# Kernel optimization log

Measured on AMD Instinct MI355X. Metric: run time of the kernel, lower is better.

Reference implementation:

```python
import jax, jax.numpy as jnp
import numpy as np

ALPHA = 0.2  # leaky relu slope
NEG_INF = -9e15  # matches torch constant -9000000000000000.0


def setup_inputs() -> dict:
    key = jax.random.key(0)
    k1, k2, k3, k4, k5 = jax.random.split(key, 5)
    B, S, FIN, FOUT, H = 1, 4096, 128, 64, 8
    input_seq = jax.random.normal(k1, (B, S, FIN), dtype=jnp.float32)
    adj = jax.random.randint(k2, (B, S, S), 0, 2, dtype=jnp.int32)
    W = jax.random.normal(k3, (H, FIN, FOUT), dtype=jnp.float32) * 0.1
    a_1 = jax.random.normal(k4, (H, FOUT, 1), dtype=jnp.float32) * 0.1
    a_2 = jax.random.normal(k5, (H, FOUT, 1), dtype=jnp.float32) * 0.1
    return {"input_seq": input_seq, "adj": adj, "W": W, "a_1": a_1, "a_2": a_2}


def reference(input_seq, adj, W, a_1, a_2):
    B, S, _ = input_seq.shape
    H, _, FOUT = W.shape
    # h: [B, H, S, FOUT]
    h = jnp.einsum('bni,hio->bhno', input_seq, W)
    f1 = jnp.einsum('bhno,hoz->bhnz', h, a_1)[..., 0]  # [B,H,S]
    f2 = jnp.einsum('bhno,hoz->bhnz', h, a_2)[..., 0]  # [B,H,S]
    # e[b,h,i,j] = f1[i] + f2[j]
    e = jax.nn.leaky_relu(f1[:, :, :, None] + f2[:, :, None, :], ALPHA)
    mask = adj[:, None, :, :] > 0  # [B,1,S,S] broadcast over heads
    e = jnp.where(mask, e, NEG_INF)
    # NOTE: original softmax is over dim=2 (source-node axis), not -1
    attention = jax.nn.softmax(e, axis=2)
    # dropout is inference-mode no-op
    node_out = jnp.einsum('bhij,bhjo->bhio', attention, h)  # [B,H,S,FOUT]
    node_out = jnp.transpose(node_out, (0, 2, 1, 3)).reshape(B, S, H * FOUT)
    node_out = jax.nn.elu(node_out)
    return jnp.squeeze(node_out)
```

## Files before the change

kernel.cpp:

```cpp
#include <hip/hip_runtime.h>

#define S 4096
#define FIN 128
#define FOUT 64
#define H 8
#define ALPHA 0.2f

typedef __attribute__((ext_vector_type(2)))  _Float16 f16x2;
typedef __attribute__((ext_vector_type(8)))  _Float16 f16x8;
typedef __attribute__((ext_vector_type(16))) float    f32x16;

__device__ __forceinline__ unsigned short f2h(float x) {
    return __builtin_bit_cast(unsigned short, (_Float16)x);
}

__global__ __launch_bounds__(256) void k_proj(const float* __restrict__ X,
                                              const float* __restrict__ W,
                                              const float* __restrict__ a1,
                                              const float* __restrict__ a2,
                                              unsigned short* __restrict__ hT,
                                              float2* __restrict__ E1h,
                                              float2* __restrict__ E2p) {
    __shared__ float xs[64][36];
    __shared__ float Ws[32][68];
    const int h  = blockIdx.y;
    const int j0 = blockIdx.x * 64;
    const int t  = threadIdx.x;
    const int fg = t & 15, rg = t >> 4;
    const int jr = t >> 2, q = t & 3;
    const int kw = t >> 3, cw = t & 7;
    float acc[4][4] = {};
#pragma unroll
    for (int k0 = 0; k0 < FIN; k0 += 32) {
        *(float4*)&xs[jr][q * 8]      = *(const float4*)&X[(j0 + jr) * FIN + k0 + q * 8];
        *(float4*)&xs[jr][q * 8 + 4]  = *(const float4*)&X[(j0 + jr) * FIN + k0 + q * 8 + 4];
        *(float4*)&Ws[kw][cw * 8]     = *(const float4*)&W[(h * FIN + k0 + kw) * FOUT + cw * 8];
        *(float4*)&Ws[kw][cw * 8 + 4] = *(const float4*)&W[(h * FIN + k0 + kw) * FOUT + cw * 8 + 4];
        __syncthreads();
#pragma unroll
        for (int kc = 0; kc < 8; ++kc) {
            float4 xr[4], wr[4];
#pragma unroll
            for (int r = 0; r < 4; ++r) xr[r] = *(const float4*)&xs[4 * rg + r][kc * 4];
#pragma unroll
            for (int kk = 0; kk < 4; ++kk) wr[kk] = *(const float4*)&Ws[kc * 4 + kk][fg * 4];
#pragma unroll
            for (int r = 0; r < 4; ++r) {
                const float* xp = (const float*)&xr[r];
#pragma unroll
                for (int kk = 0; kk < 4; ++kk) {
                    const float xv = xp[kk];
                    acc[r][0] += xv * wr[kk].x;
                    acc[r][1] += xv * wr[kk].y;
                    acc[r][2] += xv * wr[kk].z;
                    acc[r][3] += xv * wr[kk].w;
                }
            }
        }
        __syncthreads();
    }
    const float4 a1v = *(const float4*)&a1[h * FOUT + fg * 4];
    const float4 a2v = *(const float4*)&a2[h * FOUT + fg * 4];
#pragma unroll
    for (int r = 0; r < 4; ++r) {
        float p1 = acc[r][0] * a1v.x + acc[r][1] * a1v.y + acc[r][2] * a1v.z + acc[r][3] * a1v.w;
        float p2 = acc[r][0] * a2v.x + acc[r][1] * a2v.y + acc[r][2] * a2v.z + acc[r][3] * a2v.w;
#pragma unroll
        for (int off = 1; off < 16; off <<= 1) {
            p1 += __shfl_xor(p1, off, 64);
            p2 += __shfl_xor(p2, off, 64);
        }
        if (fg == 0) {
            const int row = j0 + 4 * rg + r;
            E1h[(size_t)row * H + h] = make_float2(__expf(p1), __expf(ALPHA * p1));
            E2p[h * S + row]         = make_float2(__expf(p2), __expf(ALPHA * p2));
        }
    }
#pragma unroll
    for (int c = 0; c < 4; ++c) {
        ushort4 pk;
        pk.x = f2h(acc[0][c]);
        pk.y = f2h(acc[1][c]);
        pk.z = f2h(acc[2][c]);
        pk.w = f2h(acc[3][c]);
        *(ushort4*)&hT[(h * FOUT + fg * 4 + c) * S + j0 + 4 * rg] = pk;
    }
}

__global__ __launch_bounds__(256) void k_colsum(const int* __restrict__ adj,
                                                const float2* __restrict__ E1h,
                                                const float2* __restrict__ E2p,
                                                float* __restrict__ Dcol,
                                                unsigned int* __restrict__ bm) {
    __shared__ float red[4][H][64];
    const int j0    = blockIdx.x * 64;
    const int ibase = blockIdx.y * 256;
    const int t  = threadIdx.x;
    const int jl = t & 63;
    const int wv = __builtin_amdgcn_readfirstlane(t >> 6);
    float2 e2v[H];
    float Dl[H];
#pragma unroll
    for (int hh = 0; hh < H; ++hh) { e2v[hh] = E2p[hh * S + j0 + jl]; Dl[hh] = 0.f; }
    const int rowbase = ibase + wv * 64;
    for (int s = 0; s < 64; ++s) {
        const int row = rowbase + s;
        const float2* __restrict__ e1r = E1h + (size_t)row * H;
        const int av = adj[(size_t)row * S + j0 + jl];
        const unsigned long long blt = __ballot(av != 0);
        if (jl == 0)
            *(uint2*)&bm[row * (S / 32) + (j0 >> 5)] =
                make_uint2((unsigned int)blt, (unsigned int)(blt >> 32));
        const float bf = av != 0 ? 1.f : 0.f;
#pragma unroll
        for (int hh = 0; hh < H; ++hh) {
            const float2 e1 = e1r[hh];
            Dl[hh] = fmaf(bf, fmaxf(e1.x * e2v[hh].x, e1.y * e2v[hh].y), Dl[hh]);
        }
    }
#pragma unroll
    for (int hh = 0; hh < H; ++hh) red[wv][hh][jl] = Dl[hh];
    __syncthreads();
    if (wv == 0) {
#pragma unroll
        for (int hh = 0; hh < H; ++hh) {
            const float sum = red[0][hh][jl] + red[1][hh][jl] +
                              red[2][hh][jl] + red[3][hh][jl];
            atomicAdd(&Dcol[hh * S + j0 + jl], sum);
        }
    }
}

__global__ __launch_bounds__(256) void k_finish(const float* __restrict__ Dcol,
                                                const float2* __restrict__ E2p,
                                                uint2* __restrict__ wE2h) {
    const int idx = blockIdx.x * 256 + threadIdx.x;
    const int hh = idx >> 11, p = idx & 2047;
    const int j = 2 * p;
    const float2 a  = E2p[hh * S + j];
    const float2 b  = E2p[hh * S + j + 1];
    const float  wa = 1.0f / Dcol[hh * S + j];
    const float  wb = 1.0f / Dcol[hh * S + j + 1];
    f16x2 qx, qy;
    qx[0] = (_Float16)(a.x * wa); qx[1] = (_Float16)(b.x * wb);
    qy[0] = (_Float16)(a.y * wa); qy[1] = (_Float16)(b.y * wb);
    wE2h[idx] = make_uint2(__builtin_bit_cast(unsigned int, qx),
                           __builtin_bit_cast(unsigned int, qy));
}

__global__ __launch_bounds__(512, 4) void k_attn(const unsigned int* __restrict__ bm,
                                                 const float2* __restrict__ E1h,
                                                 const uint2* __restrict__ wE2h,
                                                 const unsigned short* __restrict__ hT,
                                                 float* __restrict__ out) {
    __shared__ __align__(16) char smem[65536];
    const int h  = blockIdx.y;
    const int i0 = blockIdx.x * 64;
    const int t  = threadIdx.x;
    const int lane = t & 63, wv = t >> 6;
    const int q = wv >> 1, mw = wv & 1;
    const int am = lane & 31, kh = lane >> 5;
    const int i  = i0 + mw * 32 + am;
    const int tq = t & 127;
    const int sf = tq >> 1;
    const int sc = (tq & 1) * 4;
    unsigned short* B0 = (unsigned short*)(smem + q * 16384);
    unsigned short* B1 = B0 + 4096;
    const int jbase = q * 1024;

    const float2 e1 = E1h[(size_t)i * H + h];
    f16x2 ea2, eb2;
    ea2[0] = ea2[1] = (_Float16)e1.x;
    eb2[0] = eb2[1] = (_Float16)e1.y;

    f32x16 acc0 = {0,0,0,0,0,0,0,0,0,0,0,0,0,0,0,0};
    f32x16 acc1 = {0,0,0,0,0,0,0,0,0,0,0,0,0,0,0,0};

    const unsigned short* hrow  = hT + ((h * FOUT + sf) * S) + jbase + sc * 8;
    const unsigned int*   bmrow = bm + (size_t)i * (S / 32) + (jbase >> 5);
    const uint2*          e2b   = wE2h + h * (S / 2) + (jbase >> 1) + kh * 4;

    {
        const uint4* sp = (const uint4*)hrow;
        const uint4 v0 = sp[0], v1 = sp[1], v2 = sp[2], v3 = sp[3];
        *(uint4*)(B0 + sf * 64 + (((sc + 0) ^ (sf & 7)) * 8)) = v0;
        *(uint4*)(B0 + sf * 64 + (((sc + 1) ^ (sf & 7)) * 8)) = v1;
        *(uint4*)(B0 + sf * 64 + (((sc + 2) ^ (sf & 7)) * 8)) = v2;
        *(uint4*)(B0 + sf * 64 + (((sc + 3) ^ (sf & 7)) * 8)) = v3;
    }
    uint2 mrn = *(const uint2*)bmrow;
    __syncthreads();

    for (int jt = 0; jt < 16; ++jt) {
        unsigned short* Bc = (jt & 1) ? B1 : B0;
        unsigned short* Bn = (jt & 1) ? B0 : B1;
        const uint2 mr = mrn;
        if (jt < 15) {
            const uint4* sp = (const uint4*)(hrow + (jt + 1) * 64);
            const uint4 v0 = sp[0], v1 = sp[1], v2 = sp[2], v3 = sp[3];
            *(uint4*)(Bn + sf * 64 + (((sc + 0) ^ (sf & 7)) * 8)) = v0;
            *(uint4*)(Bn + sf * 64 + (((sc + 1) ^ (sf & 7)) * 8)) = v1;
            *(uint4*)(Bn + sf * 64 + (((sc + 2) ^ (sf & 7)) * 8)) = v2;
            *(uint4*)(Bn + sf * 64 + (((sc + 3) ^ (sf & 7)) * 8)) = v3;
            mrn = *(const uint2*)(bmrow + (jt + 1) * 2);
        }
        const unsigned int sh = kh * 8;
        unsigned int bys[4];
        bys[0] = (mr.x >> sh) & 0xffu;
        bys[1] = (mr.x >> (sh + 16)) & 0xffu;
        bys[2] = (mr.y >> sh) & 0xffu;
        bys[3] = (mr.y >> (sh + 16)) & 0xffu;
#pragma unroll
        for (int s = 0; s < 4; ++s) {
            const uint4 eA = *(const uint4*)(e2b + jt * 32 + s * 8);
            const uint4 eB = *(const uint4*)(e2b + jt * 32 + s * 8 + 2);
            const unsigned int by = bys[s];
            uint4 aw;
#define GAT_PAIR(pp, qxu, qyu, dst)                                               \
            {                                                                     \
                const f16x2 pa = ea2 * __builtin_bit_cast(f16x2, qxu);            \
                const f16x2 pb = eb2 * __builtin_bit_cast(f16x2, qyu);            \
                const unsigned int pm = __builtin_bit_cast(unsigned int,          \
                    __builtin_elementwise_max(pa, pb));                           \
                const unsigned int t2 = (by >> (2 * pp)) & 3u;                    \
                const unsigned int msk = ((0u - (t2 & 1u)) & 0xFFFFu) |           \
                                         ((0u - (t2 >> 1)) << 16);                \
                dst = pm & msk;                                                   \
            }
            GAT_PAIR(0, eA.x, eA.y, aw.x)
            GAT_PAIR(1, eA.z, eA.w, aw.y)
            GAT_PAIR(2, eB.x, eB.y, aw.z)
            GAT_PAIR(3, eB.z, eB.w, aw.w)
#undef GAT_PAIR
            const int chunk = s * 2 + kh;
            const f16x8 a  = __builtin_bit_cast(f16x8, aw);
            const f16x8 b0 = *(const f16x8*)(Bc + am * 64 + ((chunk ^ (am & 7)) * 8));
            const f16x8 b1 = *(const f16x8*)(Bc + (am + 32) * 64 + ((chunk ^ (am & 7)) * 8));
            acc0 = __builtin_amdgcn_mfma_f32_32x32x16_f16(a, b0, acc0, 0, 0, 0);
            acc1 = __builtin_amdgcn_mfma_f32_32x32x16_f16(a, b1, acc1, 0, 0, 0);
        }
        __syncthreads();
    }

    float* r1 = (float*)smem;
    float* r3 = (float*)(smem + 18432);
    const int ro = (mw * 64 + lane) * 36;
    if (q == 1) {
#pragma unroll
        for (int r = 0; r < 16; ++r) { r1[ro + r] = acc0[r]; r1[ro + 16 + r] = acc1[r]; }
    }
    if (q == 3) {
#pragma unroll
        for (int r = 0; r < 16; ++r) { r3[ro + r] = acc0[r]; r3[ro + 16 + r] = acc1[r]; }
    }
    __syncthreads();
    if (q == 0) {
#pragma unroll
        for (int r = 0; r < 16; ++r) { acc0[r] += r1[ro + r]; acc1[r] += r1[ro + 16 + r]; }
    }
    if (q == 2) {
#pragma unroll
        for (int r = 0; r < 16; ++r) { acc0[r] += r3[ro + r]; acc1[r] += r3[ro + 16 + r]; }
    }
    __syncthreads();
    if (q == 2) {
#pragma unroll
        for (int r = 0; r < 16; ++r) { r1[ro + r] = acc0[r]; r1[ro + 16 + r] = acc1[r]; }
    }
    __syncthreads();
    if (q == 0) {
#pragma unroll
        for (int r = 0; r < 16; ++r) { acc0[r] += r1[ro + r]; acc1[r] += r1[ro + 16 + r]; }
#pragma unroll
        for (int r = 0; r < 16; ++r) {
            const int il  = (r & 3) + 8 * (r >> 2) + 4 * kh;
            const int row = i0 + mw * 32 + il;
            const float x0 = acc0[r], x1 = acc1[r];
            out[row * (H * FOUT) + h * FOUT + am]      = x0 > 0.f ? x0 : __expf(x0) - 1.f;
            out[row * (H * FOUT) + h * FOUT + 32 + am] = x1 > 0.f ? x1 : __expf(x1) - 1.f;
        }
    }
}

extern "C" void kernel_launch(void* const* d_in, const int* in_sizes, int n_in,
                              void* d_out, int out_size, void* d_ws, size_t ws_size,
                              hipStream_t stream) {
    const float* X   = (const float*)d_in[0];
    const int*   adj = (const int*)d_in[1];
    const float* W   = (const float*)d_in[2];
    const float* a1  = (const float*)d_in[3];
    const float* a2  = (const float*)d_in[4];
    float* out = (float*)d_out;

    char* ws = (char*)d_ws;
    unsigned short* hT   = (unsigned short*)ws;
    float2*         E1h  = (float2*)(ws + 4194304);
    float2*         E2p  = (float2*)(ws + 4456448);
    float*          Dcol = (float*)(ws + 4718592);
    uint2*          wE2h = (uint2*)(ws + 4849664);
    unsigned int*   bm   = (unsigned int*)(ws + 4980736);

    (void)hipMemsetAsync(Dcol, 0, H * S * sizeof(float), stream);
    k_proj  <<<dim3(S / 64, H),       256, 0, stream>>>(X, W, a1, a2, hT, E1h, E2p);
    k_colsum<<<dim3(S / 64, S / 256), 256, 0, stream>>>(adj, E1h, E2p, Dcol, bm);
    k_finish<<<dim3(H * S / 512),     256, 0, stream>>>(Dcol, E2p, wE2h);
    k_attn  <<<dim3(S / 64, H),       512, 0, stream>>>(bm, E1h, wE2h, hT, out);
}
```

Baseline: 211.5 us.

## Fuse normalization into attention kernel, drop atomics, load B operands directly

Removes the memset and the k_finish kernel. k_colsum now writes per-block partial column sums instead of atomics, and k_attn reduces those 16 partials per column into shared memory at its start. The adjacency bitmask is stored transposed so each lane's mask loads coalesce across rows. The hT tile is no longer staged through double-buffered LDS with barriers; MFMA B operands are read straight from global memory with a padded row stride. This saves launches, atomics and per-tile syncs, but every attention block now redoes the normalization reduction and relies on the cache to serve the uncoalesced B-operand loads.

```diff
diff --git a/kernel.cpp b/kernel.cpp
--- a/kernel.cpp
+++ b/kernel.cpp
@@ -1,6 +1,7 @@
 #include <hip/hip_runtime.h>
 
 #define S 4096
+#define PS 4128
 #define FIN 128
 #define FOUT 64
 #define H 8
@@ -83,15 +84,15 @@
         pk.y = f2h(acc[1][c]);
         pk.z = f2h(acc[2][c]);
         pk.w = f2h(acc[3][c]);
-        *(ushort4*)&hT[(h * FOUT + fg * 4 + c) * S + j0 + 4 * rg] = pk;
+        *(ushort4*)&hT[(size_t)(h * FOUT + fg * 4 + c) * PS + j0 + 4 * rg] = pk;
     }
 }
 
 __global__ __launch_bounds__(256) void k_colsum(const int* __restrict__ adj,
                                                 const float2* __restrict__ E1h,
                                                 const float2* __restrict__ E2p,
-                                                float* __restrict__ Dcol,
-                                                unsigned int* __restrict__ bm) {
+                                                float* __restrict__ Dpart,
+                                                unsigned int* __restrict__ bmT) {
     __shared__ float red[4][H][64];
     const int j0    = blockIdx.x * 64;
     const int ibase = blockIdx.y * 256;
@@ -108,9 +109,10 @@
         const float2* __restrict__ e1r = E1h + (size_t)row * H;
         const int av = adj[(size_t)row * S + j0 + jl];
         const unsigned long long blt = __ballot(av != 0);
-        if (jl == 0)
-            *(uint2*)&bm[row * (S / 32) + (j0 >> 5)] =
-                make_uint2((unsigned int)blt, (unsigned int)(blt >> 32));
+        if (jl == 0) {
+            bmT[(j0 >> 5) * S + row]       = (unsigned int)blt;
+            bmT[((j0 >> 5) + 1) * S + row] = (unsigned int)(blt >> 32);
+        }
         const float bf = av != 0 ? 1.f : 0.f;
 #pragma unroll
         for (int hh = 0; hh < H; ++hh) {
@@ -126,46 +128,47 @@
         for (int hh = 0; hh < H; ++hh) {
             const float sum = red[0][hh][jl] + red[1][hh][jl] +
                               red[2][hh][jl] + red[3][hh][jl];
-            atomicAdd(&Dcol[hh * S + j0 + jl], sum);
-        }
-    }
-}
-
-__global__ __launch_bounds__(256) void k_finish(const float* __restrict__ Dcol,
-                                                const float2* __restrict__ E2p,
-                                                uint2* __restrict__ wE2h) {
-    const int idx = blockIdx.x * 256 + threadIdx.x;
-    const int hh = idx >> 11, p = idx & 2047;
-    const int j = 2 * p;
-    const float2 a  = E2p[hh * S + j];
-    const float2 b  = E2p[hh * S + j + 1];
-    const float  wa = 1.0f / Dcol[hh * S + j];
-    const float  wb = 1.0f / Dcol[hh * S + j + 1];
-    f16x2 qx, qy;
-    qx[0] = (_Float16)(a.x * wa); qx[1] = (_Float16)(b.x * wb);
-    qy[0] = (_Float16)(a.y * wa); qy[1] = (_Float16)(b.y * wb);
-    wE2h[idx] = make_uint2(__builtin_bit_cast(unsigned int, qx),
-                           __builtin_bit_cast(unsigned int, qy));
-}
-
-__global__ __launch_bounds__(512, 4) void k_attn(const unsigned int* __restrict__ bm,
+            Dpart[(blockIdx.y * H + hh) * S + j0 + jl] = sum;
+        }
+    }
+}
+
+__global__ __launch_bounds__(512, 4) void k_attn(const unsigned int* __restrict__ bmT,
                                                  const float2* __restrict__ E1h,
-                                                 const uint2* __restrict__ wE2h,
+                                                 const float* __restrict__ Dpart,
+                                                 const float2* __restrict__ E2p,
                                                  const unsigned short* __restrict__ hT,
                                                  float* __restrict__ out) {
-    __shared__ __align__(16) char smem[65536];
+    __shared__ __align__(16) char smem[53248];
     const int h  = blockIdx.y;
     const int i0 = blockIdx.x * 64;
     const int t  = threadIdx.x;
+
+    uint2* wE2s = (uint2*)smem;
+#pragma unroll
+    for (int u = 0; u < 4; ++u) {
+        const int pair = t * 4 + u;
+        const int j = 2 * pair;
+        float sx = 0.f, sy = 0.f;
+#pragma unroll
+        for (int z = 0; z < 16; ++z) {
+            const float2 d = *(const float2*)&Dpart[(z * H + h) * S + j];
+            sx += d.x; sy += d.y;
+        }
+        const float4 e2 = *(const float4*)&E2p[h * S + j];
+        const float wa = 1.0f / sx, wb = 1.0f / sy;
+        f16x2 qx, qy;
+        qx[0] = (_Float16)(e2.x * wa); qx[1] = (_Float16)(e2.z * wb);
+        qy[0] = (_Float16)(e2.y * wa); qy[1] = (_Float16)(e2.w * wb);
+        wE2s[pair] = make_uint2(__builtin_bit_cast(unsigned int, qx),
+                                __builtin_bit_cast(unsigned int, qy));
+    }
+    __syncthreads();
+
     const int lane = t & 63, wv = t >> 6;
     const int q = wv >> 1, mw = wv & 1;
     const int am = lane & 31, kh = lane >> 5;
     const int i  = i0 + mw * 32 + am;
-    const int tq = t & 127;
-    const int sf = tq >> 1;
-    const int sc = (tq & 1) * 4;
-    unsigned short* B0 = (unsigned short*)(smem + q * 16384);
-    unsigned short* B1 = B0 + 4096;
     const int jbase = q * 1024;
 
     const float2 e1 = E1h[(size_t)i * H + h];
@@ -176,44 +179,27 @@
     f32x16 acc0 = {0,0,0,0,0,0,0,0,0,0,0,0,0,0,0,0};
     f32x16 acc1 = {0,0,0,0,0,0,0,0,0,0,0,0,0,0,0,0};
 
-    const unsigned short* hrow  = hT + ((h * FOUT + sf) * S) + jbase + sc * 8;
-    const unsigned int*   bmrow = bm + (size_t)i * (S / 32) + (jbase >> 5);
-    const uint2*          e2b   = wE2h + h * (S / 2) + (jbase >> 1) + kh * 4;
-
-    {
-        const uint4* sp = (const uint4*)hrow;
-        const uint4 v0 = sp[0], v1 = sp[1], v2 = sp[2], v3 = sp[3];
-        *(uint4*)(B0 + sf * 64 + (((sc + 0) ^ (sf & 7)) * 8)) = v0;
-        *(uint4*)(B0 + sf * 64 + (((sc + 1) ^ (sf & 7)) * 8)) = v1;
-        *(uint4*)(B0 + sf * 64 + (((sc + 2) ^ (sf & 7)) * 8)) = v2;
-        *(uint4*)(B0 + sf * 64 + (((sc + 3) ^ (sf & 7)) * 8)) = v3;
-    }
-    uint2 mrn = *(const uint2*)bmrow;
-    __syncthreads();
+    const unsigned short* b0p = hT + (size_t)(h * FOUT + am) * PS + jbase;
+    const unsigned short* b1p = hT + (size_t)(h * FOUT + am + 32) * PS + jbase;
+    const unsigned int* bmcol = bmT + (jbase >> 5) * S + i;
+    const uint2* e2s = wE2s + (jbase >> 1) + kh * 4;
+    const unsigned int sh = kh * 8;
 
     for (int jt = 0; jt < 16; ++jt) {
-        unsigned short* Bc = (jt & 1) ? B1 : B0;
-        unsigned short* Bn = (jt & 1) ? B0 : B1;
-        const uint2 mr = mrn;
-        if (jt < 15) {
-            const uint4* sp = (const uint4*)(hrow + (jt + 1) * 64);
-            const uint4 v0 = sp[0], v1 = sp[1], v2 = sp[2], v3 = sp[3];
-            *(uint4*)(Bn + sf * 64 + (((sc + 0) ^ (sf & 7)) * 8)) = v0;
-            *(uint4*)(Bn + sf * 64 + (((sc + 1) ^ (sf & 7)) * 8)) = v1;
-            *(uint4*)(Bn + sf * 64 + (((sc + 2) ^ (sf & 7)) * 8)) = v2;
-            *(uint4*)(Bn + sf * 64 + (((sc + 3) ^ (sf & 7)) * 8)) = v3;
-            mrn = *(const uint2*)(bmrow + (jt + 1) * 2);
-        }
-        const unsigned int sh = kh * 8;
+        const unsigned int w0 = bmcol[(2 * jt) * S];
+        const unsigned int w1 = bmcol[(2 * jt + 1) * S];
         unsigned int bys[4];
-        bys[0] = (mr.x >> sh) & 0xffu;
-        bys[1] = (mr.x >> (sh + 16)) & 0xffu;
-        bys[2] = (mr.y >> sh) & 0xffu;
-        bys[3] = (mr.y >> (sh + 16)) & 0xffu;
+        bys[0] = (w0 >> sh) & 0xffu;
+        bys[1] = (w0 >> (sh + 16)) & 0xffu;
+        bys[2] = (w1 >> sh) & 0xffu;
+        bys[3] = (w1 >> (sh + 16)) & 0xffu;
 #pragma unroll
         for (int s = 0; s < 4; ++s) {
-            const uint4 eA = *(const uint4*)(e2b + jt * 32 + s * 8);
-            const uint4 eB = *(const uint4*)(e2b + jt * 32 + s * 8 + 2);
+            const int ko = jt * 64 + s * 16 + kh * 8;
+            const f16x8 b0 = *(const f16x8*)(b0p + ko);
+            const f16x8 b1 = *(const f16x8*)(b1p + ko);
+            const uint4 eA = *(const uint4*)(e2s + jt * 32 + s * 8);
+            const uint4 eB = *(const uint4*)(e2s + jt * 32 + s * 8 + 2);
             const unsigned int by = bys[s];
             uint4 aw;
 #define GAT_PAIR(pp, qxu, qyu, dst)                                               \
@@ -232,18 +218,15 @@
             GAT_PAIR(2, eB.x, eB.y, aw.z)
             GAT_PAIR(3, eB.z, eB.w, aw.w)
 #undef GAT_PAIR
-            const int chunk = s * 2 + kh;
-            const f16x8 a  = __builtin_bit_cast(f16x8, aw);
-            const f16x8 b0 = *(const f16x8*)(Bc + am * 64 + ((chunk ^ (am & 7)) * 8));
-            const f16x8 b1 = *(const f16x8*)(Bc + (am + 32) * 64 + ((chunk ^ (am & 7)) * 8));
+            const f16x8 a = __builtin_bit_cast(f16x8, aw);
             acc0 = __builtin_amdgcn_mfma_f32_32x32x16_f16(a, b0, acc0, 0, 0, 0);
             acc1 = __builtin_amdgcn_mfma_f32_32x32x16_f16(a, b1, acc1, 0, 0, 0);
         }
-        __syncthreads();
-    }
-
-    float* r1 = (float*)smem;
-    float* r3 = (float*)(smem + 18432);
+    }
+    __syncthreads();
+
+    float* r1 = (float*)(smem + 16384);
+    float* r3 = (float*)(smem + 16384 + 18432);
     const int ro = (mw * 64 + lane) * 36;
     if (q == 1) {
 #pragma unroll
@@ -294,15 +277,12 @@
 
     char* ws = (char*)d_ws;
     unsigned short* hT   = (unsigned short*)ws;
-    float2*         E1h  = (float2*)(ws + 4194304);
-    float2*         E2p  = (float2*)(ws + 4456448);
-    float*          Dcol = (float*)(ws + 4718592);
-    uint2*          wE2h = (uint2*)(ws + 4849664);
-    unsigned int*   bm   = (unsigned int*)(ws + 4980736);
-
-    (void)hipMemsetAsync(Dcol, 0, H * S * sizeof(float), stream);
+    float2*         E1h  = (float2*)(ws + 4325376);
+    float2*         E2p  = (float2*)(ws + 4587520);
+    float*          Dpart= (float*)(ws + 4849664);
+    unsigned int*   bmT  = (unsigned int*)(ws + 6946816);
+
     k_proj  <<<dim3(S / 64, H),       256, 0, stream>>>(X, W, a1, a2, hT, E1h, E2p);
-    k_colsum<<<dim3(S / 64, S / 256), 256, 0, stream>>>(adj, E1h, E2p, Dcol, bm);
-    k_finish<<<dim3(H * S / 512),     256, 0, stream>>>(Dcol, E2p, wE2h);
-    k_attn  <<<dim3(S / 64, H),       512, 0, stream>>>(bm, E1h, wE2h, hT, out);
-}
+    k_colsum<<<dim3(S / 64, S / 256), 256, 0, stream>>>(adj, E1h, E2p, Dpart, bmT);
+    k_attn  <<<dim3(S / 64, H),       512, 0, stream>>>(bmT, E1h, Dpart, E2p, hT, out);
+}
```

Result: no change. 211.2 us (-0.1%).
